# Kernel tuning notes

Measured on AMD Instinct MI355X. Metric: run time of the kernel, lower is better.

## Reference

```python
import jax, jax.numpy as jnp
import numpy as np

ALPHA = 0.2        # LeakyReLU negative slope used in standard GAT
NEG_INF = -9e15    # mask fill value from the canonical pyGAT implementation


def _gat_layer(x, adj_mask, W, a1, a2, concat):
    """One GAT attention head.
    x: [B,N,Din], adj_mask: [B,N,N] bool, W: [Din,Dout], a1/a2: [Dout].
    """
    Wh = jnp.einsum('bnd,df->bnf', x, W)               # [B,N,Dout]
    f1 = jnp.einsum('bnf,f->bn', Wh, a1)               # source scores
    f2 = jnp.einsum('bnf,f->bn', Wh, a2)               # target scores
    e = jax.nn.leaky_relu(f1[:, :, None] + f2[:, None, :], ALPHA)  # [B,N,N]
    e = jnp.where(adj_mask, e, jnp.float32(NEG_INF))
    attn = jax.nn.softmax(e, axis=-1)                  # masked row-softmax
    out = jnp.einsum('bnm,bmf->bnf', attn, Wh)         # neighbor aggregation
    return jax.nn.elu(out) if concat else out


def setup_inputs() -> dict:
    key = jax.random.key(0)
    ks = jax.random.split(key, 8)
    B, N, Din, Dout, H = 32, 512, 768, 256, 8
    x = jax.random.normal(ks[0], (B, N, Din), jnp.float32)
    adj = jax.random.randint(ks[1], (B, N, N), 0, 2, jnp.int32)  # {0,1} adjacency
    W0 = jax.random.normal(ks[2], (H, Din, Dout), jnp.float32) * (1.0 / np.sqrt(Din))
    a1_0 = jax.random.normal(ks[3], (H, Dout), jnp.float32) * 0.1
    a2_0 = jax.random.normal(ks[4], (H, Dout), jnp.float32) * 0.1
    Wo = jax.random.normal(ks[5], (Dout, Dout), jnp.float32) * (1.0 / np.sqrt(Dout))
    a1_o = jax.random.normal(ks[6], (Dout,), jnp.float32) * 0.1
    a2_o = jax.random.normal(ks[7], (Dout,), jnp.float32) * 0.1
    return dict(x=x, adj=adj, W0=W0, a1_0=a1_0, a2_0=a2_0,
                Wo=Wo, a1_o=a1_o, a2_o=a2_o)


def reference(x, adj, W0, a1_0, a2_0, Wo, a1_o, a2_o):
    mask = adj > 0
    # multi-head layer: vmap over heads replaces the Python head loop
    heads = jax.vmap(lambda W, a1, a2: _gat_layer(x, mask, W, a1, a2, True))(
        W0, a1_0, a2_0)                                # [H,B,N,Dout]
    h = heads.mean(axis=0)                             # cat+unsqueeze+mean(dim=1)
    # dropout is identity in eval mode (p effectively 0 for the baseline)
    out = _gat_layer(h, mask, Wo, a1_o, a2_o, False)   # gat_out, concat=False
    return jax.nn.relu(out)                            # [B,N,Dout]
```

## Files before the change

kernel.cpp:

```cpp
#include <hip/hip_runtime.h>
#include <hip/hip_bf16.h>
#include <stdint.h>

typedef __bf16 bf16;
typedef short short8 __attribute__((ext_vector_type(8)));
typedef float f32x4 __attribute__((ext_vector_type(4)));

#define LOG2E 1.4426950408889634f

union V16 { uint4 u; short8 s; bf16 h[8]; };
union U8  { ushort4 s; bf16 h[4]; };

typedef const __attribute__((address_space(1))) void* gp_t;
typedef __attribute__((address_space(3))) void* lp_t;
__device__ __forceinline__ void gld16(const bf16* g, bf16* l) {
  __builtin_amdgcn_global_load_lds((gp_t)g, (lp_t)l, 16, 0, 0);
}

__global__ __launch_bounds__(256) void k_zero(float4* __restrict__ p, int n4) {
  int i = blockIdx.x * 256 + threadIdx.x;
  if (i < n4) p[i] = {0.f, 0.f, 0.f, 0.f};
}

__global__ __launch_bounds__(256) void k_cvt(const float* __restrict__ src,
                                             bf16* __restrict__ dst, long long n) {
  long long i = ((long long)blockIdx.x * 256 + threadIdx.x) * 8;
  if (i >= n) return;
  float4 a = *(const float4*)(src + i);
  float4 b = *(const float4*)(src + i + 4);
  U8 w0, w1;
  w0.h[0] = (bf16)a.x; w0.h[1] = (bf16)a.y; w0.h[2] = (bf16)a.z; w0.h[3] = (bf16)a.w;
  w1.h[0] = (bf16)b.x; w1.h[1] = (bf16)b.y; w1.h[2] = (bf16)b.z; w1.h[3] = (bf16)b.w;
  *(ushort4*)(dst + i)     = w0.s;
  *(ushort4*)(dst + i + 4) = w1.s;
}

__global__ __launch_bounds__(256) void k_maskpack(const int* __restrict__ adj,
                                                  unsigned long long* __restrict__ mask) {
  int wid = blockIdx.x * 4 + (threadIdx.x >> 6);
  int lane = threadIdx.x & 63;
  int a = adj[(long long)wid * 64 + lane];
  unsigned long long m = __ballot(a > 0);
  if (lane == 0) mask[wid] = m;
}

__global__ __launch_bounds__(256) void k_transpose(const float* __restrict__ src,
                                                   bf16* __restrict__ dst, int R, int C) {
  __shared__ float t[32][33];
  int c0 = blockIdx.x * 32, r0 = blockIdx.y * 32;
  src += (long long)blockIdx.z * R * C;
  dst += (long long)blockIdx.z * R * C;
  int tx = threadIdx.x & 31, ty = threadIdx.x >> 5;
  for (int rr = ty; rr < 32; rr += 8)
    t[rr][tx] = src[(long long)(r0 + rr) * C + (c0 + tx)];
  __syncthreads();
  for (int cc = ty; cc < 32; cc += 8)
    dst[(long long)(c0 + cc) * R + (r0 + tx)] = (bf16)t[tx][cc];
}

__global__ __launch_bounds__(256) void k_gemm(const bf16* __restrict__ A,
                                              const bf16* __restrict__ WT,
                                              bf16* __restrict__ outT, int K,
                                              const float* __restrict__ a1,
                                              const float* __restrict__ a2,
                                              int aStride,
                                              float* __restrict__ f1out,
                                              float* __restrict__ f2out) {
  __shared__ bf16 As[128 * 32];
  __shared__ bf16 Bs[128 * 32];
  const int nb = blockIdx.x, mb = blockIdx.y, h = blockIdx.z;
  const int tid = threadIdx.x, wave = tid >> 6, lane = tid & 63;
  const int lrow = lane & 15, quad = lane >> 4;
  const long long mbase = (long long)mb * 128;
  const int nbase = nb * 128;
  const bf16* W = WT + (long long)h * 256 * K;
  const int wm = (wave >> 1) * 64, wn = (wave & 1) * 64;
  const int srow = wave * 16 + (lane >> 2);
  const int skoff = (lane & 3) * 8;
  const bf16* ag0 = A + (mbase + srow) * K + skoff;
  const bf16* ag1 = ag0 + 64 * K;
  const bf16* bg0 = W + (long long)(nbase + srow) * K + skoff;
  const bf16* bg1 = bg0 + 64 * K;
  bf16* lA0 = As + wave * 16 * 32;
  bf16* lA1 = As + (64 + wave * 16) * 32;
  bf16* lB0 = Bs + wave * 16 * 32;
  bf16* lB1 = Bs + (64 + wave * 16) * 32;
  f32x4 acc[4][4];
#pragma unroll
  for (int i = 0; i < 4; i++)
#pragma unroll
    for (int j = 0; j < 4; j++) acc[i][j] = {0.f, 0.f, 0.f, 0.f};
  for (int k0 = 0; k0 < K; k0 += 32) {
    __syncthreads();
    gld16(ag0 + k0, lA0);
    gld16(ag1 + k0, lA1);
    gld16(bg0 + k0, lB0);
    gld16(bg1 + k0, lB1);
    __syncthreads();
    V16 af[4], bfx[4];
#pragma unroll
    for (int mi = 0; mi < 4; mi++)
      af[mi].u = *(const uint4*)(As + (wm + mi * 16 + lrow) * 32 + quad * 8);
#pragma unroll
    for (int ni = 0; ni < 4; ni++)
      bfx[ni].u = *(const uint4*)(Bs + (wn + ni * 16 + lrow) * 32 + quad * 8);
#pragma unroll
    for (int mi = 0; mi < 4; mi++)
#pragma unroll
      for (int ni = 0; ni < 4; ni++)
        acc[mi][ni] = __builtin_amdgcn_mfma_f32_16x16x32_bf16(af[mi].s, bfx[ni].s, acc[mi][ni], 0, 0, 0);
  }
#pragma unroll
  for (int mi = 0; mi < 4; mi++) {
    long long m0 = mbase + wm + mi * 16 + quad * 4;
    int bbi = (int)(m0 >> 9);
    int jj = (int)(m0 & 511);
    int js = jj >> 5, qp = (jj >> 3) & 3, eo = jj & 7;
    long long rowbase = (long long)(h * 32 + bbi) * 131072 +
                        (long long)js * 512 + (qp * 16 + lrow) * 8 + eo;
#pragma unroll
    for (int ni = 0; ni < 4; ni++) {
      int ft = ((nbase + wn) >> 4) + ni;
      U8 w;
#pragma unroll
      for (int r = 0; r < 4; r++) w.h[r] = (bf16)acc[mi][ni][r];
      *(ushort4*)(outT + rowbase + (long long)ft * 8192) = w.s;
    }
  }
  float av1[4], av2[4];
#pragma unroll
  for (int ni = 0; ni < 4; ni++) {
    int f = nbase + wn + ni * 16 + lrow;
    av1[ni] = a1[h * aStride + f];
    av2[ni] = a2[h * aStride + f];
  }
#pragma unroll
  for (int mi = 0; mi < 4; mi++) {
#pragma unroll
    for (int r = 0; r < 4; r++) {
      float s1 = 0.f, s2 = 0.f;
#pragma unroll
      for (int ni = 0; ni < 4; ni++) {
        s1 = __builtin_fmaf(acc[mi][ni][r], av1[ni], s1);
        s2 = __builtin_fmaf(acc[mi][ni][r], av2[ni], s2);
      }
#pragma unroll
      for (int off = 1; off < 16; off <<= 1) {
        s1 += __shfl_xor(s1, off);
        s2 += __shfl_xor(s2, off);
      }
      if (lrow == 0) {
        long long m0 = mbase + wm + mi * 16 + quad * 4 + r;
        atomicAdd(&f1out[(long long)h * 16384 + m0], s1);
        atomicAdd(&f2out[(long long)h * 16384 + m0], s2);
      }
    }
  }
}

__global__ __launch_bounds__(256) void k_passA(const float* __restrict__ f1p,
                                               const float* __restrict__ f2p,
                                               const unsigned long long* __restrict__ mask,
                                               float* __restrict__ cc) {
  const int hb = blockIdx.x, bb = hb & 31;
  const int wave = threadIdx.x >> 6, lane = threadIdx.x & 63;
  const int i = blockIdx.y * 4 + wave;
  const float* f2 = f2p + hb * 512;
  float4 va = *(const float4*)(f2 + lane * 8);
  float4 vb = *(const float4*)(f2 + lane * 8 + 4);
  float vj[8] = {va.x, va.y, va.z, va.w, vb.x, vb.y, vb.z, vb.w};
  unsigned int mb = ((const unsigned char*)(mask + ((long long)bb * 512 + i) * 8))[lane];
  float f1 = f1p[hb * 512 + i];
  float m = -INFINITY;
#pragma unroll
  for (int t = 0; t < 8; t++)
    if ((mb >> t) & 1) m = fmaxf(m, vj[t]);
#pragma unroll
  for (int off = 32; off; off >>= 1) m = fmaxf(m, __shfl_xor(m, off));
  float s = f1 + m;
  float M2 = LOG2E * fmaxf(s, 0.2f * s);
  float d = 0.f;
#pragma unroll
  for (int t = 0; t < 8; t++) {
    float e0 = f1 + vj[t];
    float e = fmaxf(e0, 0.2f * e0);
    float p = exp2f(__builtin_fmaf(LOG2E, e, -M2));
    d += ((mb >> t) & 1) ? p : 0.f;
  }
#pragma unroll
  for (int off = 32; off; off >>= 1) d += __shfl_xor(d, off);
  if (lane == 0) {
    float cv = M2 + log2f(d);
    if (!isfinite(M2) || !(d > 0.f)) cv = INFINITY;
    cc[hb * 512 + i] = cv;
  }
}

__device__ __forceinline__ int pchunk(int row, int c) {
  return row * 512 + (((c + 3 * row) & 63) << 3);
}

template <int NSPLIT, int NHB, int ROWS, int MODE>
__global__ __launch_bounds__(256) void k_pv(const bf16* __restrict__ WhT,
                                            const float* __restrict__ f1p,
                                            const float* __restrict__ cc,
                                            const float* __restrict__ f2p,
                                            const unsigned long long* __restrict__ mask,
                                            void* __restrict__ out0,
                                            void* __restrict__ out1) {
  constexpr int TPR = 256 / ROWS;
  constexpr int NT  = 64 / TPR;
  constexpr int MI  = ROWS / 16;
  constexpr int RB  = 32 * (512 / ROWS);
  constexpr int CPT = 256 / TPR;
  __shared__ union { bf16 P[ROWS * 512]; float hs[ROWS * 264]; } sh;
  __shared__ unsigned char ms[ROWS * 64];
  const int id = blockIdx.x;
  const int hp = id / RB;
  const int rid = id % RB;
  const int bb = rid & 31, it = rid >> 5;
  const int ibase = it * ROWS;
  const int tid = threadIdx.x, wave = tid >> 6, lane = tid & 63;
  const int lrow = lane & 15, quad = lane >> 4;
  const int pi = tid / TPR;
  const int pj = tid % TPR;
  {
    const uint4* msrc = (const uint4*)(mask + ((long long)bb * 512 + ibase) * 8);
    if (tid < ROWS * 4) ((uint4*)ms)[tid] = msrc[tid];
  }
  __syncthreads();
  unsigned long long mreg = 0;
#pragma unroll
  for (int t = 0; t < NT; t++)
    mreg |= (unsigned long long)ms[pi * 64 + pj + t * TPR] << (t * 8);
  f32x4 hacc[MI][4];
#pragma unroll
  for (int i = 0; i < MI; i++)
#pragma unroll
    for (int j = 0; j < 4; j++) hacc[i][j] = {0.f, 0.f, 0.f, 0.f};

  auto buildP = [&](int h) {
    const int hb = h * 32 + bb;
    const float f1v = f1p[hb * 512 + ibase + pi];
    const float cv  = cc[hb * 512 + ibase + pi];
    const float Ac = __builtin_fmaf(LOG2E, f1v, -cv);
    const float Bc = __builtin_fmaf(0.2f * LOG2E, f1v, -cv);
    const float* f2 = f2p + hb * 512;
#pragma unroll
    for (int t = 0; t < NT; t++) {
      const int ch = pj + t * TPR;
      const int j0 = ch * 8;
      float4 u0 = *(const float4*)(f2 + j0);
      float4 u1 = *(const float4*)(f2 + j0 + 4);
      float fj[8] = {u0.x, u0.y, u0.z, u0.w, u1.x, u1.y, u1.z, u1.w};
      unsigned int mb = (unsigned int)(mreg >> (t * 8)) & 0xff;
      V16 pk;
#pragma unroll
      for (int u = 0; u < 8; u++) {
        float e = fmaxf(__builtin_fmaf(LOG2E, fj[u], Ac),
                        __builtin_fmaf(0.2f * LOG2E, fj[u], Bc));
        float p = ((mb >> u) & 1) ? exp2f(e) : 0.f;
        pk.h[u] = (bf16)p;
      }
      *(uint4*)(sh.P + pchunk(pi, ch)) = pk.u;
    }
  };

#pragma unroll 1
  for (int hh = 0; hh < NHB; hh++) {
    const int h = hp * NHB + hh;
    const int hb = h * 32 + bb;
    __syncthreads();
    buildP(h);
    __syncthreads();
    const bf16* wfb = WhT + (long long)hb * 131072 + (long long)wave * 32768 + lane * 8;
    f32x4 acc[MI][4];
#pragma unroll
    for (int i = 0; i < MI; i++)
#pragma unroll
      for (int j = 0; j < 4; j++) acc[i][j] = {0.f, 0.f, 0.f, 0.f};
#pragma unroll
    for (int js = 0; js < 16; js++) {
      V16 af[MI], bfr[4];
#pragma unroll
      for (int mi = 0; mi < MI; mi++)
        af[mi].u = *(const uint4*)(sh.P + pchunk(mi * 16 + lrow, js * 4 + quad));
#pragma unroll
      for (int ni = 0; ni < 4; ni++)
        bfr[ni].u = *(const uint4*)(wfb + ni * 8192 + js * 512);
#pragma unroll
      for (int ni = 0; ni < 4; ni++)
#pragma unroll
        for (int mi = 0; mi < MI; mi++)
          acc[mi][ni] = __builtin_amdgcn_mfma_f32_16x16x32_bf16(af[mi].s, bfr[ni].s, acc[mi][ni], 0, 0, 0);
    }
#pragma unroll
    for (int mi = 0; mi < MI; mi++)
#pragma unroll
      for (int ni = 0; ni < 4; ni++)
#pragma unroll
        for (int r = 0; r < 4; r++) {
          float v = acc[mi][ni][r];
          hacc[mi][ni][r] += (MODE == 1) ? v
                           : (v > 0.f ? v : (exp2f(v * LOG2E) - 1.f));
        }
  }
  __syncthreads();
#pragma unroll
  for (int mi = 0; mi < MI; mi++)
#pragma unroll
    for (int ni = 0; ni < 4; ni++) {
      int f = wave * 64 + ni * 16 + lrow;
#pragma unroll
      for (int r = 0; r < 4; r++) {
        int row = mi * 16 + quad * 4 + r;
        sh.hs[row * 264 + f] = hacc[mi][ni][r];
      }
    }
  __syncthreads();
  const int fb = pj * CPT;
  float* op = (float*)(hp ? out1 : out0) +
              (((long long)bb * 512) + ibase + pi) * 256 + fb;
#pragma unroll
  for (int c0 = 0; c0 < CPT; c0 += 4) {
    float4 w;
    w.x = sh.hs[pi * 264 + fb + c0 + 0];
    w.y = sh.hs[pi * 264 + fb + c0 + 1];
    w.z = sh.hs[pi * 264 + fb + c0 + 2];
    w.w = sh.hs[pi * 264 + fb + c0 + 3];
    if (MODE == 1) {
      w.x = fmaxf(w.x, 0.f); w.y = fmaxf(w.y, 0.f);
      w.z = fmaxf(w.z, 0.f); w.w = fmaxf(w.w, 0.f);
    }
    *(float4*)(op + c0) = w;
  }
}

__global__ __launch_bounds__(256) void k_fin(const float* __restrict__ a,
                                             const float* __restrict__ b,
                                             bf16* __restrict__ dst) {
  long long i = ((long long)blockIdx.x * 256 + threadIdx.x) * 4;
  float4 x = *(const float4*)(a + i);
  float4 y = *(const float4*)(b + i);
  U8 w;
  w.h[0] = (bf16)((x.x + y.x) * 0.125f);
  w.h[1] = (bf16)((x.y + y.y) * 0.125f);
  w.h[2] = (bf16)((x.z + y.z) * 0.125f);
  w.h[3] = (bf16)((x.w + y.w) * 0.125f);
  *(ushort4*)(dst + i) = w.s;
}

extern "C" void kernel_launch(void* const* d_in, const int* in_sizes, int n_in,
                              void* d_out, int out_size, void* d_ws, size_t ws_size,
                              hipStream_t stream) {
  const float* x    = (const float*)d_in[0];
  const int*   adj  = (const int*)d_in[1];
  const float* W0   = (const float*)d_in[2];
  const float* a1_0 = (const float*)d_in[3];
  const float* a2_0 = (const float*)d_in[4];
  const float* Wo   = (const float*)d_in[5];
  const float* a1_o = (const float*)d_in[6];
  const float* a2_o = (const float*)d_in[7];

  char* p = (char*)d_ws;
  auto take = [&](size_t n) { char* r = p; p += (n + 255) & ~(size_t)255; return r; };
  unsigned long long* maskb = (unsigned long long*)take(32ull * 512 * 8 * 8);
  bf16*  xb   = (bf16*)take(32ull * 512 * 768 * 2);
  bf16*  W0T  = (bf16*)take(8ull * 256 * 768 * 2);
  bf16*  WoT  = (bf16*)take(256ull * 256 * 2);
  bf16*  WhT  = (bf16*)take(8ull * 32 * 256 * 512 * 2);
  float* f1p1 = (float*)take(8ull * 32 * 512 * 4);
  float* f2p1 = (float*)take(8ull * 32 * 512 * 4);
  float* f1p2 = (float*)take(32ull * 512 * 4);
  float* f2p2 = (float*)take(32ull * 512 * 4);
  float* c1   = (float*)take(8ull * 32 * 512 * 4);
  float* c2   = (float*)take(32ull * 512 * 4);
  float* pv1  = (float*)take(32ull * 512 * 256 * 4);
  float* pv0  = (float*)xb;
  bf16*  hmid = (bf16*)((char*)xb + 16ull * 1024 * 1024);
  bf16*  Wh2T = WhT;

  k_zero<<<288, 256, 0, stream>>>((float4*)f1p1, 73728);
  k_cvt<<<6144, 256, 0, stream>>>(x, xb, 32ll * 512 * 768);
  k_maskpack<<<32768, 256, 0, stream>>>(adj, maskb);
  k_transpose<<<dim3(8, 24, 8), 256, 0, stream>>>(W0, W0T, 768, 256);
  k_transpose<<<dim3(8, 8, 1), 256, 0, stream>>>(Wo, WoT, 256, 256);
  k_gemm<<<dim3(2, 128, 8), 256, 0, stream>>>(xb, W0T, WhT, 768,
                                              a1_0, a2_0, 256, f1p1, f2p1);
  k_passA<<<dim3(256, 128), 256, 0, stream>>>(f1p1, f2p1, maskb, c1);
  k_pv<2, 4, 16, 0><<<2048, 256, 0, stream>>>(WhT, f1p1, c1, f2p1, maskb, pv0, pv1);
  k_fin<<<4096, 256, 0, stream>>>(pv0, pv1, hmid);
  k_gemm<<<dim3(2, 128, 1), 256, 0, stream>>>(hmid, WoT, Wh2T, 256,
                                              a1_o, a2_o, 0, f1p2, f2p2);
  k_passA<<<dim3(32, 128), 256, 0, stream>>>(f1p2, f2p2, maskb, c2);
  k_pv<1, 1, 16, 1><<<1024, 256, 0, stream>>>(Wh2T, f1p2, c2, f2p2, maskb, d_out, nullptr);
}
```

Baseline: 401.7 us.

## Build attention probabilities in registers, one wave per block in PV

Replaces the 256-thread PV kernel, which staged probability tiles and outputs through shared memory with barriers, by a single-wave kernel. Each wave builds its 16-row probability fragment directly in MFMA A-operand registers and covers half of the feature dimension. This removes LDS traffic and __syncthreads, and writes results straight from the accumulators. In exchange, the probability exp work is duplicated across the two feature-half blocks, and output stores become strided scalar writes. Register pressure also rises from holding 16 packed fragments.

```diff
diff --git a/kernel.cpp b/kernel.cpp
--- a/kernel.cpp
+++ b/kernel.cpp
@@ -196,144 +196,95 @@
   }
 }
 
-__device__ __forceinline__ int pchunk(int row, int c) {
-  return row * 512 + (((c + 3 * row) & 63) << 3);
-}
-
-template <int NSPLIT, int NHB, int ROWS, int MODE>
-__global__ __launch_bounds__(256) void k_pv(const bf16* __restrict__ WhT,
+template <int NSPLIT, int NHB, int MODE>
+__global__ __launch_bounds__(64) void k_pvr(const bf16* __restrict__ WhT,
                                             const float* __restrict__ f1p,
                                             const float* __restrict__ cc,
                                             const float* __restrict__ f2p,
                                             const unsigned long long* __restrict__ mask,
                                             void* __restrict__ out0,
                                             void* __restrict__ out1) {
-  constexpr int TPR = 256 / ROWS;
-  constexpr int NT  = 64 / TPR;
-  constexpr int MI  = ROWS / 16;
-  constexpr int RB  = 32 * (512 / ROWS);
-  constexpr int CPT = 256 / TPR;
-  __shared__ union { bf16 P[ROWS * 512]; float hs[ROWS * 264]; } sh;
-  __shared__ unsigned char ms[ROWS * 64];
   const int id = blockIdx.x;
-  const int hp = id / RB;
-  const int rid = id % RB;
-  const int bb = rid & 31, it = rid >> 5;
-  const int ibase = it * ROWS;
-  const int tid = threadIdx.x, wave = tid >> 6, lane = tid & 63;
+  const int bb = id & 31;
+  const int it = (id >> 5) & 31;
+  const int t2 = id >> 10;
+  const int fh = t2 & 1;
+  const int hp = t2 >> 1;
+  const int ibase = it * 16;
+  const int lane = threadIdx.x;
   const int lrow = lane & 15, quad = lane >> 4;
-  const int pi = tid / TPR;
-  const int pj = tid % TPR;
+
+  unsigned int mw[16];
   {
-    const uint4* msrc = (const uint4*)(mask + ((long long)bb * 512 + ibase) * 8);
-    if (tid < ROWS * 4) ((uint4*)ms)[tid] = msrc[tid];
-  }
-  __syncthreads();
-  unsigned long long mreg = 0;
-#pragma unroll
-  for (int t = 0; t < NT; t++)
-    mreg |= (unsigned long long)ms[pi * 64 + pj + t * TPR] << (t * 8);
-  f32x4 hacc[MI][4];
-#pragma unroll
-  for (int i = 0; i < MI; i++)
-#pragma unroll
-    for (int j = 0; j < 4; j++) hacc[i][j] = {0.f, 0.f, 0.f, 0.f};
-
-  auto buildP = [&](int h) {
+    const uint4* mrow = (const uint4*)(mask + ((long long)bb * 512 + ibase + lrow) * 8);
+    uint4 a0 = mrow[0], a1 = mrow[1], a2 = mrow[2], a3 = mrow[3];
+    mw[0] = a0.x;  mw[1] = a0.y;  mw[2] = a0.z;  mw[3] = a0.w;
+    mw[4] = a1.x;  mw[5] = a1.y;  mw[6] = a1.z;  mw[7] = a1.w;
+    mw[8] = a2.x;  mw[9] = a2.y;  mw[10] = a2.z; mw[11] = a2.w;
+    mw[12] = a3.x; mw[13] = a3.y; mw[14] = a3.z; mw[15] = a3.w;
+  }
+
+  f32x4 hacc[8];
+#pragma unroll
+  for (int ni = 0; ni < 8; ni++) hacc[ni] = {0.f, 0.f, 0.f, 0.f};
+
+#pragma unroll 1
+  for (int hh = 0; hh < NHB; hh++) {
+    const int h = hp * NHB + hh;
     const int hb = h * 32 + bb;
-    const float f1v = f1p[hb * 512 + ibase + pi];
-    const float cv  = cc[hb * 512 + ibase + pi];
+    const float f1v = f1p[hb * 512 + ibase + lrow];
+    const float cv  = cc[hb * 512 + ibase + lrow];
     const float Ac = __builtin_fmaf(LOG2E, f1v, -cv);
     const float Bc = __builtin_fmaf(0.2f * LOG2E, f1v, -cv);
-    const float* f2 = f2p + hb * 512;
-#pragma unroll
-    for (int t = 0; t < NT; t++) {
-      const int ch = pj + t * TPR;
-      const int j0 = ch * 8;
+    const float* f2 = f2p + (long long)hb * 512;
+    V16 pa[16];
+#pragma unroll
+    for (int js = 0; js < 16; js++) {
+      const int j0 = js * 32 + quad * 8;
       float4 u0 = *(const float4*)(f2 + j0);
       float4 u1 = *(const float4*)(f2 + j0 + 4);
       float fj[8] = {u0.x, u0.y, u0.z, u0.w, u1.x, u1.y, u1.z, u1.w};
-      unsigned int mb = (unsigned int)(mreg >> (t * 8)) & 0xff;
-      V16 pk;
+      unsigned int mb = (mw[js] >> (quad * 8)) & 0xffu;
 #pragma unroll
       for (int u = 0; u < 8; u++) {
         float e = fmaxf(__builtin_fmaf(LOG2E, fj[u], Ac),
                         __builtin_fmaf(0.2f * LOG2E, fj[u], Bc));
         float p = ((mb >> u) & 1) ? exp2f(e) : 0.f;
-        pk.h[u] = (bf16)p;
-      }
-      *(uint4*)(sh.P + pchunk(pi, ch)) = pk.u;
-    }
-  };
-
-#pragma unroll 1
-  for (int hh = 0; hh < NHB; hh++) {
-    const int h = hp * NHB + hh;
-    const int hb = h * 32 + bb;
-    __syncthreads();
-    buildP(h);
-    __syncthreads();
-    const bf16* wfb = WhT + (long long)hb * 131072 + (long long)wave * 32768 + lane * 8;
-    f32x4 acc[MI][4];
-#pragma unroll
-    for (int i = 0; i < MI; i++)
-#pragma unroll
-      for (int j = 0; j < 4; j++) acc[i][j] = {0.f, 0.f, 0.f, 0.f};
+        pa[js].h[u] = (bf16)p;
+      }
+    }
+    const bf16* wfb = WhT + (long long)hb * 131072 + (long long)fh * 65536 + lane * 8;
+    f32x4 acc[8];
+#pragma unroll
+    for (int ni = 0; ni < 8; ni++) acc[ni] = {0.f, 0.f, 0.f, 0.f};
 #pragma unroll
     for (int js = 0; js < 16; js++) {
-      V16 af[MI], bfr[4];
-#pragma unroll
-      for (int mi = 0; mi < MI; mi++)
-        af[mi].u = *(const uint4*)(sh.P + pchunk(mi * 16 + lrow, js * 4 + quad));
-#pragma unroll
-      for (int ni = 0; ni < 4; ni++)
-        bfr[ni].u = *(const uint4*)(wfb + ni * 8192 + js * 512);
-#pragma unroll
-      for (int ni = 0; ni < 4; ni++)
-#pragma unroll
-        for (int mi = 0; mi < MI; mi++)
-          acc[mi][ni] = __builtin_amdgcn_mfma_f32_16x16x32_bf16(af[mi].s, bfr[ni].s, acc[mi][ni], 0, 0, 0);
-    }
-#pragma unroll
-    for (int mi = 0; mi < MI; mi++)
-#pragma unroll
-      for (int ni = 0; ni < 4; ni++)
-#pragma unroll
-        for (int r = 0; r < 4; r++) {
-          float v = acc[mi][ni][r];
-          hacc[mi][ni][r] += (MODE == 1) ? v
-                           : (v > 0.f ? v : (exp2f(v * LOG2E) - 1.f));
-        }
-  }
-  __syncthreads();
-#pragma unroll
-  for (int mi = 0; mi < MI; mi++)
-#pragma unroll
-    for (int ni = 0; ni < 4; ni++) {
-      int f = wave * 64 + ni * 16 + lrow;
+#pragma unroll
+      for (int ni = 0; ni < 8; ni++) {
+        V16 b;
+        b.u = *(const uint4*)(wfb + ni * 8192 + js * 512);
+        acc[ni] = __builtin_amdgcn_mfma_f32_16x16x32_bf16(pa[js].s, b.s, acc[ni], 0, 0, 0);
+      }
+    }
+#pragma unroll
+    for (int ni = 0; ni < 8; ni++)
 #pragma unroll
       for (int r = 0; r < 4; r++) {
-        int row = mi * 16 + quad * 4 + r;
-        sh.hs[row * 264 + f] = hacc[mi][ni][r];
-      }
-    }
-  __syncthreads();
-  const int fb = pj * CPT;
+        float v = acc[ni][r];
+        hacc[ni][r] += (MODE == 1) ? v
+                     : (v > 0.f ? v : (exp2f(v * LOG2E) - 1.f));
+      }
+  }
   float* op = (float*)(hp ? out1 : out0) +
-              (((long long)bb * 512) + ibase + pi) * 256 + fb;
-#pragma unroll
-  for (int c0 = 0; c0 < CPT; c0 += 4) {
-    float4 w;
-    w.x = sh.hs[pi * 264 + fb + c0 + 0];
-    w.y = sh.hs[pi * 264 + fb + c0 + 1];
-    w.z = sh.hs[pi * 264 + fb + c0 + 2];
-    w.w = sh.hs[pi * 264 + fb + c0 + 3];
-    if (MODE == 1) {
-      w.x = fmaxf(w.x, 0.f); w.y = fmaxf(w.y, 0.f);
-      w.z = fmaxf(w.z, 0.f); w.w = fmaxf(w.w, 0.f);
-    }
-    *(float4*)(op + c0) = w;
-  }
+              ((long long)bb * 512 + ibase) * 256 + fh * 128;
+#pragma unroll
+  for (int ni = 0; ni < 8; ni++)
+#pragma unroll
+    for (int r = 0; r < 4; r++) {
+      float v = hacc[ni][r];
+      if (MODE == 1) v = fmaxf(v, 0.f);
+      op[(quad * 4 + r) * 256 + ni * 16 + lrow] = v;
+    }
 }
 
 __global__ __launch_bounds__(256) void k_fin(const float* __restrict__ a,
@@ -388,10 +339,10 @@
   k_gemm<<<dim3(2, 128, 8), 256, 0, stream>>>(xb, W0T, WhT, 768,
                                               a1_0, a2_0, 256, f1p1, f2p1);
   k_passA<<<dim3(256, 128), 256, 0, stream>>>(f1p1, f2p1, maskb, c1);
-  k_pv<2, 4, 16, 0><<<2048, 256, 0, stream>>>(WhT, f1p1, c1, f2p1, maskb, pv0, pv1);
+  k_pvr<2, 4, 0><<<4096, 64, 0, stream>>>(WhT, f1p1, c1, f2p1, maskb, pv0, pv1);
   k_fin<<<4096, 256, 0, stream>>>(pv0, pv1, hmid);
   k_gemm<<<dim3(2, 128, 1), 256, 0, stream>>>(hmid, WoT, Wh2T, 256,
                                               a1_o, a2_o, 0, f1p2, f2p2);
   k_passA<<<dim3(32, 128), 256, 0, stream>>>(f1p2, f2p2, maskb, c2);
-  k_pv<1, 1, 16, 1><<<1024, 256, 0, stream>>>(Wh2T, f1p2, c2, f2p2, maskb, d_out, nullptr);
-}
+  k_pvr<1, 1, 1><<<2048, 64, 0, stream>>>(Wh2T, f1p2, c2, f2p2, maskb, d_out, nullptr);
+}
```

Result: slower. 617.7 us (+53.7%).
